# Kernel optimization log

Hardware: AMD Instinct MI355X
Metric: run time of the kernel (lower is better)

Reference implementation:

```python
import jax, jax.numpy as jnp
import numpy as np

B, S, D, H = 32, 1024, 512, 512  # batch, seq_len, input_size, hidden_size


def _init_dir_params(key, D, H):
    # Gate order along the stacked 4H axis: i, f, o, c (matches NaiveLSTM gates)
    k = jax.random.split(key, 4)
    s_in = 1.0 / np.sqrt(D)
    s_h = 1.0 / np.sqrt(H)
    Wx = jax.random.uniform(k[0], (4 * H, D), jnp.float32, -s_in, s_in)
    Wh = jax.random.uniform(k[1], (4 * H, H), jnp.float32, -s_h, s_h)
    bx = jax.random.uniform(k[2], (4 * H,), jnp.float32, -s_in, s_in)
    bh = jax.random.uniform(k[3], (4 * H,), jnp.float32, -s_h, s_h)
    # torch code sets W_f.bias and U_f.bias to 1.0 (forget-gate slice = index 1)
    bx = bx.at[H:2 * H].set(1.0)
    bh = bh.at[H:2 * H].set(1.0)
    return Wx, Wh, bx, bh


def setup_inputs() -> dict:
    key = jax.random.key(0)
    kx, kf, kb = jax.random.split(key, 3)
    x = jax.random.normal(kx, (B, S, D), jnp.float32)
    Wx_f, Wh_f, bx_f, bh_f = _init_dir_params(kf, D, H)
    Wx_b, Wh_b, bx_b, bh_b = _init_dir_params(kb, D, H)
    return {"x": x, "Wx_f": Wx_f, "Wh_f": Wh_f, "bx_f": bx_f, "bh_f": bh_f,
            "Wx_b": Wx_b, "Wh_b": Wh_b, "bx_b": bx_b, "bh_b": bh_b}


def _run_lstm(x_seq, Wx, Wh, bx, bh):
    # x_seq: [B, S, D]; returns (hs [B,S,H], h_final [B,H], c_final [B,H])
    b = x_seq.shape[0]
    h_dim = Wh.shape[1]
    # one big GEMM for all input-to-hidden projections (fused across gates & time)
    xg = jnp.einsum('bsd,gd->bsg', x_seq, Wx) + bx  # [B, S, 4H]

    def step(carry, xg_t):
        h, c = carry
        g = xg_t + h @ Wh.T + bh  # [B, 4H]
        i, f, o, ct = jnp.split(g, 4, axis=-1)
        c_new = jax.nn.sigmoid(f) * c + jax.nn.sigmoid(i) * jnp.tanh(ct)
        h_new = jax.nn.sigmoid(o) * jnp.tanh(c_new)
        return (h_new, c_new), h_new

    init = (jnp.zeros((b, h_dim), x_seq.dtype), jnp.zeros((b, h_dim), x_seq.dtype))
    (hN, cN), hs = jax.lax.scan(step, init, jnp.swapaxes(xg, 0, 1))
    return jnp.swapaxes(hs, 0, 1), hN, cN


def reference(x, Wx_f, Wh_f, bx_f, bh_f, Wx_b, Wh_b, bx_b, bh_b):
    out_f, hF, cF = _run_lstm(x, Wx_f, Wh_f, bx_f, bh_f)
    # backward direction: scan over time-reversed sequence, then un-reverse
    out_b_rev, hB, cB = _run_lstm(x[:, ::-1], Wx_b, Wh_b, bx_b, bh_b)
    out_b = out_b_rev[:, ::-1]
    outputs = jnp.concatenate([out_f, out_b], axis=-1)  # dropout p=0.0 -> identity
    final_hidden = jnp.concatenate([hF, hB], axis=-1)
    final_cell = jnp.concatenate([cF, cB], axis=-1)
    return outputs, final_hidden, final_cell
```

## Files before the change

kernel.cpp:

```cpp
#include <hip/hip_runtime.h>

typedef unsigned short u16;
typedef unsigned int u32;
typedef unsigned long long u64;
typedef __attribute__((ext_vector_type(8))) short short8v;
typedef __attribute__((ext_vector_type(8))) __bf16 bf16x8;
typedef __attribute__((ext_vector_type(4))) float f32x4;
typedef __attribute__((ext_vector_type(2))) float f32x2;

#define AS1 __attribute__((address_space(1)))
#define AS3 __attribute__((address_space(3)))

__device__ __forceinline__ u16 f2bf(float f) {
  unsigned u = __float_as_uint(f);
  u += 0x7fffu + ((u >> 16) & 1u);
  return (u16)(u >> 16);
}
__device__ __forceinline__ float bf2f(u16 h) {
  return __uint_as_float(((unsigned)h) << 16);
}
__device__ __forceinline__ void gload_lds16(const void* g, void* l) {
  __builtin_amdgcn_global_load_lds((const AS1 void*)g, (AS3 void*)l, 16, 0, 0);
}
__device__ __forceinline__ bf16x8 ld8(const u16* p) {
  return __builtin_bit_cast(bf16x8, *reinterpret_cast<const short8v*>(p));
}
__device__ __forceinline__ float sigf(float x) { return 1.0f / (1.0f + __expf(-x)); }
__device__ __forceinline__ float tanhfast(float x) {
  float e = __expf(2.0f * x);
  return 1.0f - 2.0f / (e + 1.0f);
}

__global__ __launch_bounds__(256) void k_conv_x(const float* __restrict__ x,
                                                u16* __restrict__ xh) {
  int i = blockIdx.x * 256 + threadIdx.x;
  float4 v = reinterpret_cast<const float4*>(x)[i];
  ushort4 o;
  o.x = f2bf(v.x); o.y = f2bf(v.y); o.z = f2bf(v.z); o.w = f2bf(v.w);
  reinterpret_cast<ushort4*>(xh)[i] = o;
}

__global__ __launch_bounds__(256) void k_pack_w(
    const float* __restrict__ Wx_f, const float* __restrict__ Wh_f,
    const float* __restrict__ bx_f, const float* __restrict__ bh_f,
    const float* __restrict__ Wx_b, const float* __restrict__ Wh_b,
    const float* __restrict__ bx_b, const float* __restrict__ bh_b,
    u16* __restrict__ wall, u16* __restrict__ whp, float* __restrict__ bias) {
  int i = blockIdx.x * 256 + threadIdx.x;
  int np = i >> 7;
  int k4 = i & 127;
  int d  = np >> 11;
  int p  = np & 2047;
  int src = (p & 3) * 512 + (p >> 2);
  const float* wx = d ? Wx_b : Wx_f;
  const float* wh = d ? Wh_b : Wh_f;
  float4 vx = reinterpret_cast<const float4*>(wx + (size_t)src * 512)[k4];
  float4 vh = reinterpret_cast<const float4*>(wh + (size_t)src * 512)[k4];
  ushort4 ox, oh;
  ox.x = f2bf(vx.x); ox.y = f2bf(vx.y); ox.z = f2bf(vx.z); ox.w = f2bf(vx.w);
  oh.x = f2bf(vh.x); oh.y = f2bf(vh.y); oh.z = f2bf(vh.z); oh.w = f2bf(vh.w);
  reinterpret_cast<ushort4*>(wall + (size_t)np * 512)[k4] = ox;
  reinterpret_cast<ushort4*>(whp  + (size_t)np * 512)[k4] = oh;
  if (k4 == 0) bias[np] = d ? (bx_b[src] + bh_b[src]) : (bx_f[src] + bh_f[src]);
}

template <bool XGBF16>
__global__ __launch_bounds__(256) void k_gemm_xg(
    const u16* __restrict__ A, const u16* __restrict__ Bw,
    const float* __restrict__ bias,
    float* __restrict__ Cf, u16* __restrict__ Ch) {
  __shared__ __align__(16) u16 lA[128 * 32];
  __shared__ __align__(16) u16 lB[128 * 32];
  const int tid  = threadIdx.x;
  const int lane = tid & 63;
  const int w    = tid >> 6;
  const int wr   = w >> 1, wc = w & 1;
  const size_t brow = (size_t)blockIdx.y * 128;
  const int    bcol = blockIdx.x * 128;

  f32x4 acc[4][4] = {};

  for (int kk = 0; kk < 16; ++kk) {
    const int k0 = kk * 32;
    __syncthreads();
#pragma unroll
    for (int q = 0; q < 2; ++q) {
      int idx = q * 256 + tid;
      int row = idx >> 2, c = idx & 3;
      gload_lds16(A  + (brow + row) * 512 + k0 + c * 8, &lA[idx * 8]);
      gload_lds16(Bw + (size_t)(bcol + row) * 512 + k0 + c * 8, &lB[idx * 8]);
    }
    __syncthreads();

    bf16x8 af[4], bfr[4];
#pragma unroll
    for (int m = 0; m < 4; ++m) {
      int row = wr * 64 + m * 16 + (lane & 15);
      af[m] = ld8(&lA[row * 32 + (lane >> 4) * 8]);
    }
#pragma unroll
    for (int n = 0; n < 4; ++n) {
      int row = wc * 64 + n * 16 + (lane & 15);
      bfr[n] = ld8(&lB[row * 32 + (lane >> 4) * 8]);
    }
#pragma unroll
    for (int m = 0; m < 4; ++m)
#pragma unroll
      for (int n = 0; n < 4; ++n)
        acc[m][n] = __builtin_amdgcn_mfma_f32_16x16x32_bf16(af[m], bfr[n], acc[m][n], 0, 0, 0);
  }

#pragma unroll
  for (int m = 0; m < 4; ++m) {
#pragma unroll
    for (int n = 0; n < 4; ++n) {
      int col = bcol + wc * 64 + n * 16 + (lane & 15);
      float bb = bias[col];
#pragma unroll
      for (int r = 0; r < 4; ++r) {
        size_t row = brow + wr * 64 + m * 16 + (lane >> 4) * 4 + r;
        float v = acc[m][n][r] + bb;
        if (XGBF16) Ch[row * 4096 + col] = f2bf(v);
        else        Cf[row * 4096 + col] = v;
      }
    }
  }
}

template <bool XGBF16>
__global__ __launch_bounds__(256, 1) void k_rnn(
    const u16* __restrict__ whp,
    const float* __restrict__ xgf, const u16* __restrict__ xgh,
    u32* __restrict__ hbuf, u32* __restrict__ flags,
    float* __restrict__ out, float* __restrict__ fh, float* __restrict__ fc) {
  const int tid  = threadIdx.x;
  const int lane = tid & 63;
  const int w    = tid >> 6;
  const int bid  = (int)blockIdx.x;
  const int d     = bid >> 4;
  const int ntile = bid & 15;

  __shared__ __align__(16) u16 hlds[32 * 512];
  __shared__ __align__(16) float gbuf[32][132];

  const u16* wbase = whp + (size_t)(d * 2048 + ntile * 128 + w * 32) * 512;
  bf16x8 wf[16][2];
#pragma unroll
  for (int kk = 0; kk < 16; ++kk)
#pragma unroll
    for (int n = 0; n < 2; ++n)
      wf[kk][n] = ld8(wbase + (size_t)(n * 16 + (lane & 15)) * 512 + kk * 32 + (lane >> 4) * 8);

  const int brow = tid >> 4;
  const int jp   = tid & 15;
  const int colbase = d * 2048 + ntile * 128 + jp * 8;
  const int r0 = lane & 15;
  const int qb = lane >> 4;
  const int swz = r0 & 7;

  float cst[2][2] = {{0.f, 0.f}, {0.f, 0.f}};

  const int FSTR = 64;
  u32* myflag = flags + (d * 16 + ntile) * FSTR;
  const u32* spinflag = flags + (d * 16 + ((tid & 127) >> 3)) * FSTR;

  for (int t = 0; t < 1024; ++t) {
    const int sd = d ? (1023 - t) : t;

    short8v xh0, xh1;
    f32x4 xf0a, xf0b, xf1a, xf1b;
    {
      size_t xoff0 = ((size_t)(brow * 1024 + sd)) * 4096 + colbase;
      size_t xoff1 = ((size_t)((16 + brow) * 1024 + sd)) * 4096 + colbase;
      if (XGBF16) {
        xh0 = *reinterpret_cast<const short8v*>(xgh + xoff0);
        xh1 = *reinterpret_cast<const short8v*>(xgh + xoff1);
      } else {
        xf0a = *reinterpret_cast<const f32x4*>(xgf + xoff0);
        xf0b = *reinterpret_cast<const f32x4*>(xgf + xoff0 + 4);
        xf1a = *reinterpret_cast<const f32x4*>(xgf + xoff1);
        xf1b = *reinterpret_cast<const f32x4*>(xgf + xoff1 + 4);
      }
    }

    if (t > 0) {
      while (__hip_atomic_load(spinflag, __ATOMIC_RELAXED, __HIP_MEMORY_SCOPE_AGENT) < (u32)t)
        __builtin_amdgcn_s_sleep(1);
      asm volatile("" ::: "memory");
    }

    const u64* hg = (const u64*)hbuf + ((size_t)(t & 1) * 2 + d) * 4096;
    u64 hv[16];
#pragma unroll
    for (int p = 0; p < 16; ++p)
      hv[p] = __hip_atomic_load(hg + p * 256 + tid, __ATOMIC_RELAXED, __HIP_MEMORY_SCOPE_AGENT);

    {
      char* hb = (char*)hlds;
#pragma unroll
      for (int p = 0; p < 16; ++p) {
        int idx = p * 256 + tid;
        int b = idx >> 7, jq = idx & 127;
        *(u64*)(hb + b * 1024 + (((jq >> 1) ^ (b & 7)) << 4) + ((jq & 1) << 3)) = hv[p];
      }
    }
    __syncthreads();

    f32x4 acc[2][2] = {};
    {
      const char* hbc = (const char*)hlds;
#pragma unroll
      for (int kk = 0; kk < 16; ++kk) {
        int u0 = (((kk * 4 + qb) ^ swz) << 4);
        bf16x8 a0 = *(const bf16x8*)(hbc + r0 * 1024 + u0);
        bf16x8 a1 = *(const bf16x8*)(hbc + (16 + r0) * 1024 + u0);
#pragma unroll
        for (int n = 0; n < 2; ++n) {
          acc[0][n] = __builtin_amdgcn_mfma_f32_16x16x32_bf16(a0, wf[kk][n], acc[0][n], 0, 0, 0);
          acc[1][n] = __builtin_amdgcn_mfma_f32_16x16x32_bf16(a1, wf[kk][n], acc[1][n], 0, 0, 0);
        }
      }
    }

#pragma unroll
    for (int m = 0; m < 2; ++m)
#pragma unroll
      for (int n = 0; n < 2; ++n)
#pragma unroll
        for (int r = 0; r < 4; ++r)
          gbuf[m * 16 + qb * 4 + r][w * 32 + n * 16 + r0] = acc[m][n][r];
    __syncthreads();

    u32* hdst = hbuf + ((size_t)((t + 1) & 1) * 2 + d) * 8192;
    u32 pk[2];
    float hh[2][2];
#pragma unroll
    for (int it = 0; it < 2; ++it) {
      int b = it * 16 + brow;
      float4 g0 = *reinterpret_cast<const float4*>(&gbuf[b][jp * 8]);
      float4 g1 = *reinterpret_cast<const float4*>(&gbuf[b][jp * 8 + 4]);
      float xi0, xff0, xo0, xc0, xi1, xff1, xo1, xc1;
      if (XGBF16) {
        const short8v& xv = it ? xh1 : xh0;
        xi0 = bf2f((u16)xv[0]); xff0 = bf2f((u16)xv[1]);
        xo0 = bf2f((u16)xv[2]); xc0  = bf2f((u16)xv[3]);
        xi1 = bf2f((u16)xv[4]); xff1 = bf2f((u16)xv[5]);
        xo1 = bf2f((u16)xv[6]); xc1  = bf2f((u16)xv[7]);
      } else {
        const f32x4& va = it ? xf1a : xf0a;
        const f32x4& vb = it ? xf1b : xf0b;
        xi0 = va[0]; xff0 = va[1]; xo0 = va[2]; xc0 = va[3];
        xi1 = vb[0]; xff1 = vb[1]; xo1 = vb[2]; xc1 = vb[3];
      }
      float gi0 = g0.x + xi0, gf0 = g0.y + xff0, go0 = g0.z + xo0, gc0 = g0.w + xc0;
      float gi1 = g1.x + xi1, gf1 = g1.y + xff1, go1 = g1.z + xo1, gc1 = g1.w + xc1;
      float cn0 = sigf(gf0) * cst[it][0] + sigf(gi0) * tanhfast(gc0);
      float cn1 = sigf(gf1) * cst[it][1] + sigf(gi1) * tanhfast(gc1);
      float hn0 = sigf(go0) * tanhfast(cn0);
      float hn1 = sigf(go1) * tanhfast(cn1);
      cst[it][0] = cn0; cst[it][1] = cn1;
      pk[it] = (u32)f2bf(hn0) | ((u32)f2bf(hn1) << 16);
      hh[it][0] = hn0; hh[it][1] = hn1;
    }

#pragma unroll
    for (int it = 0; it < 2; ++it) {
      int b = it * 16 + brow;
      __hip_atomic_store(hdst + b * 256 + ntile * 16 + jp, pk[it],
                         __ATOMIC_RELAXED, __HIP_MEMORY_SCOPE_AGENT);
    }
    asm volatile("s_waitcnt vmcnt(0)" ::: "memory");
    __syncthreads();
    if (tid == 0)
      __hip_atomic_store(myflag, (u32)(t + 1), __ATOMIC_RELAXED, __HIP_MEMORY_SCOPE_AGENT);

#pragma unroll
    for (int it = 0; it < 2; ++it) {
      int b = it * 16 + brow;
      f32x2 ov; ov.x = hh[it][0]; ov.y = hh[it][1];
      __builtin_nontemporal_store(ov, reinterpret_cast<f32x2*>(
          out + ((size_t)(b * 1024 + sd)) * 1024 + d * 512 + ntile * 32 + jp * 2));
      if (t == 1023) {
        int fo = b * 1024 + d * 512 + ntile * 32 + jp * 2;
        f32x2 hv2; hv2.x = hh[it][0]; hv2.y = hh[it][1];
        f32x2 cv2; cv2.x = cst[it][0]; cv2.y = cst[it][1];
        *reinterpret_cast<f32x2*>(fh + fo) = hv2;
        *reinterpret_cast<f32x2*>(fc + fo) = cv2;
      }
    }
  }
}

extern "C" void kernel_launch(void* const* d_in, const int* in_sizes, int n_in,
                              void* d_out, int out_size, void* d_ws, size_t ws_size,
                              hipStream_t stream) {
  (void)in_sizes; (void)n_in; (void)out_size;
  const float* x    = (const float*)d_in[0];
  const float* Wx_f = (const float*)d_in[1];
  const float* Wh_f = (const float*)d_in[2];
  const float* bx_f = (const float*)d_in[3];
  const float* bh_f = (const float*)d_in[4];
  const float* Wx_b = (const float*)d_in[5];
  const float* Wh_b = (const float*)d_in[6];
  const float* bx_b = (const float*)d_in[7];
  const float* bh_b = (const float*)d_in[8];

  char* ws = (char*)d_ws;
  const size_t XG_F32 = (size_t)32768 * 4096 * 4;
  const size_t XG_BF  = (size_t)32768 * 4096 * 2;
  const size_t REST   = 33554432 + 4194304 + 4194304 + 16384 + 262144 + 16384;
  const bool xg_bf16 = (ws_size < XG_F32 + REST);

  size_t off = xg_bf16 ? XG_BF : XG_F32;
  float* xg_f = (float*)ws;
  u16*   xg_h = (u16*)ws;
  u16*   xh   = (u16*)(ws + off);  off += 33554432;
  u16*   wall = (u16*)(ws + off);  off += 4194304;
  u16*   whp  = (u16*)(ws + off);  off += 4194304;
  float* bias = (float*)(ws + off); off += 16384;
  u32*   hbuf = (u32*)(ws + off);  off += 262144;
  u32*   flags = (u32*)(ws + off); off += 16384;

  float* out = (float*)d_out;
  float* fh  = out + (size_t)33554432;
  float* fc  = fh + 32768;

  hipError_t e = hipMemsetAsync(hbuf, 0, 262144 + 16384, stream);
  (void)e;
  k_conv_x<<<16384, 256, 0, stream>>>(x, xh);
  k_pack_w<<<2048, 256, 0, stream>>>(Wx_f, Wh_f, bx_f, bh_f,
                                     Wx_b, Wh_b, bx_b, bh_b, wall, whp, bias);
  if (xg_bf16) {
    k_gemm_xg<true><<<dim3(32, 256), 256, 0, stream>>>(xh, wall, bias, nullptr, xg_h);
    k_rnn<true><<<32, 256, 0, stream>>>(whp, nullptr, xg_h, hbuf, flags, out, fh, fc);
  } else {
    k_gemm_xg<false><<<dim3(32, 256), 256, 0, stream>>>(xh, wall, bias, xg_f, nullptr);
    k_rnn<false><<<32, 256, 0, stream>>>(whp, xg_f, nullptr, hbuf, flags, out, fh, fc);
  }
}
```

Measured before the change: 3.820 ms.

## Replace flag-based step sync with sentinel-valued triple-buffered hidden state polling

Drops the per-block flag counters and instead triple-buffers the hidden state in global memory, filling unwritten slots with a sentinel pattern that consumers poll until every value is valid. Each wave now loads its MFMA A-fragments straight from global memory into registers, which removes the LDS staging and one barrier per step. A producer clears the buffer two steps ahead. The aim is to shorten the per-timestep cross-block handoff latency, at the cost of redundant global reads (each wave reads the full 32x512 h), higher register pressure from 64 u64 values, and a theoretical false sentinel match on a real bf16 pair.

```diff
diff --git a/kernel.cpp b/kernel.cpp
--- a/kernel.cpp
+++ b/kernel.cpp
@@ -7,9 +7,13 @@
 typedef __attribute__((ext_vector_type(8))) __bf16 bf16x8;
 typedef __attribute__((ext_vector_type(4))) float f32x4;
 typedef __attribute__((ext_vector_type(2))) float f32x2;
+typedef __attribute__((ext_vector_type(2))) u64 u64x2;
 
 #define AS1 __attribute__((address_space(1)))
 #define AS3 __attribute__((address_space(3)))
+
+#define SENT32 0x7F7F7F7Fu
+#define SENT64 0x7F7F7F7F7F7F7F7FULL
 
 __device__ __forceinline__ u16 f2bf(float f) {
   unsigned u = __float_as_uint(f);
@@ -131,7 +135,7 @@
 __global__ __launch_bounds__(256, 1) void k_rnn(
     const u16* __restrict__ whp,
     const float* __restrict__ xgf, const u16* __restrict__ xgh,
-    u32* __restrict__ hbuf, u32* __restrict__ flags,
+    u32* __restrict__ hbuf3,
     float* __restrict__ out, float* __restrict__ fh, float* __restrict__ fc) {
   const int tid  = threadIdx.x;
   const int lane = tid & 63;
@@ -140,29 +144,25 @@
   const int d     = bid >> 4;
   const int ntile = bid & 15;
 
-  __shared__ __align__(16) u16 hlds[32 * 512];
   __shared__ __align__(16) float gbuf[32][132];
 
   const u16* wbase = whp + (size_t)(d * 2048 + ntile * 128 + w * 32) * 512;
+  const int r0 = lane & 15;
+  const int qb = lane >> 4;
   bf16x8 wf[16][2];
 #pragma unroll
   for (int kk = 0; kk < 16; ++kk)
 #pragma unroll
     for (int n = 0; n < 2; ++n)
-      wf[kk][n] = ld8(wbase + (size_t)(n * 16 + (lane & 15)) * 512 + kk * 32 + (lane >> 4) * 8);
+      wf[kk][n] = ld8(wbase + (size_t)(n * 16 + r0) * 512 + kk * 32 + qb * 8);
 
   const int brow = tid >> 4;
   const int jp   = tid & 15;
   const int colbase = d * 2048 + ntile * 128 + jp * 8;
-  const int r0 = lane & 15;
-  const int qb = lane >> 4;
-  const int swz = r0 & 7;
 
   float cst[2][2] = {{0.f, 0.f}, {0.f, 0.f}};
 
-  const int FSTR = 64;
-  u32* myflag = flags + (d * 16 + ntile) * FSTR;
-  const u32* spinflag = flags + (d * 16 + ((tid & 127) >> 3)) * FSTR;
+  const int fragbase = r0 * 128 + qb * 2;
 
   for (int t = 0; t < 1024; ++t) {
     const int sd = d ? (1023 - t) : t;
@@ -183,42 +183,47 @@
       }
     }
 
-    if (t > 0) {
-      while (__hip_atomic_load(spinflag, __ATOMIC_RELAXED, __HIP_MEMORY_SCOPE_AGENT) < (u32)t)
-        __builtin_amdgcn_s_sleep(1);
-      asm volatile("" ::: "memory");
-    }
-
-    const u64* hg = (const u64*)hbuf + ((size_t)(t & 1) * 2 + d) * 4096;
-    u64 hv[16];
-#pragma unroll
-    for (int p = 0; p < 16; ++p)
-      hv[p] = __hip_atomic_load(hg + p * 256 + tid, __ATOMIC_RELAXED, __HIP_MEMORY_SCOPE_AGENT);
+    const u64* hb = (const u64*)hbuf3 + ((size_t)(t % 3) * 2 + d) * 4096;
+    u64 hv[64];
+    for (;;) {
+#pragma unroll
+      for (int kk = 0; kk < 16; ++kk) {
+        hv[kk * 2]          = __hip_atomic_load(hb + fragbase + kk * 8,
+                                  __ATOMIC_RELAXED, __HIP_MEMORY_SCOPE_AGENT);
+        hv[kk * 2 + 1]      = __hip_atomic_load(hb + fragbase + kk * 8 + 1,
+                                  __ATOMIC_RELAXED, __HIP_MEMORY_SCOPE_AGENT);
+        hv[32 + kk * 2]     = __hip_atomic_load(hb + 2048 + fragbase + kk * 8,
+                                  __ATOMIC_RELAXED, __HIP_MEMORY_SCOPE_AGENT);
+        hv[32 + kk * 2 + 1] = __hip_atomic_load(hb + 2048 + fragbase + kk * 8 + 1,
+                                  __ATOMIC_RELAXED, __HIP_MEMORY_SCOPE_AGENT);
+      }
+      int ok = 1;
+#pragma unroll
+      for (int i = 0; i < 64; ++i) {
+        u32 lo = (u32)hv[i], hi = (u32)(hv[i] >> 32);
+        ok &= (lo != SENT32) & (hi != SENT32);
+      }
+      if (ok) break;
+      __builtin_amdgcn_s_sleep(1);
+    }
 
     {
-      char* hb = (char*)hlds;
-#pragma unroll
-      for (int p = 0; p < 16; ++p) {
-        int idx = p * 256 + tid;
-        int b = idx >> 7, jq = idx & 127;
-        *(u64*)(hb + b * 1024 + (((jq >> 1) ^ (b & 7)) << 4) + ((jq & 1) << 3)) = hv[p];
-      }
-    }
-    __syncthreads();
+      u64* clr = (u64*)hbuf3 + ((size_t)((t + 2) % 3) * 2 + d) * 4096
+                 + ntile * 256 + tid;
+      __hip_atomic_store(clr, SENT64, __ATOMIC_RELAXED, __HIP_MEMORY_SCOPE_AGENT);
+    }
 
     f32x4 acc[2][2] = {};
-    {
-      const char* hbc = (const char*)hlds;
-#pragma unroll
-      for (int kk = 0; kk < 16; ++kk) {
-        int u0 = (((kk * 4 + qb) ^ swz) << 4);
-        bf16x8 a0 = *(const bf16x8*)(hbc + r0 * 1024 + u0);
-        bf16x8 a1 = *(const bf16x8*)(hbc + (16 + r0) * 1024 + u0);
-#pragma unroll
-        for (int n = 0; n < 2; ++n) {
-          acc[0][n] = __builtin_amdgcn_mfma_f32_16x16x32_bf16(a0, wf[kk][n], acc[0][n], 0, 0, 0);
-          acc[1][n] = __builtin_amdgcn_mfma_f32_16x16x32_bf16(a1, wf[kk][n], acc[1][n], 0, 0, 0);
-        }
+#pragma unroll
+    for (int kk = 0; kk < 16; ++kk) {
+      u64x2 t0; t0[0] = hv[kk * 2];      t0[1] = hv[kk * 2 + 1];
+      u64x2 t1; t1[0] = hv[32 + kk * 2]; t1[1] = hv[32 + kk * 2 + 1];
+      bf16x8 a0 = __builtin_bit_cast(bf16x8, t0);
+      bf16x8 a1 = __builtin_bit_cast(bf16x8, t1);
+#pragma unroll
+      for (int n = 0; n < 2; ++n) {
+        acc[0][n] = __builtin_amdgcn_mfma_f32_16x16x32_bf16(a0, wf[kk][n], acc[0][n], 0, 0, 0);
+        acc[1][n] = __builtin_amdgcn_mfma_f32_16x16x32_bf16(a1, wf[kk][n], acc[1][n], 0, 0, 0);
       }
     }
 
@@ -231,7 +236,6 @@
           gbuf[m * 16 + qb * 4 + r][w * 32 + n * 16 + r0] = acc[m][n][r];
     __syncthreads();
 
-    u32* hdst = hbuf + ((size_t)((t + 1) & 1) * 2 + d) * 8192;
     u32 pk[2];
     float hh[2][2];
 #pragma unroll
@@ -262,17 +266,18 @@
       pk[it] = (u32)f2bf(hn0) | ((u32)f2bf(hn1) << 16);
       hh[it][0] = hn0; hh[it][1] = hn1;
     }
-
-#pragma unroll
-    for (int it = 0; it < 2; ++it) {
-      int b = it * 16 + brow;
-      __hip_atomic_store(hdst + b * 256 + ntile * 16 + jp, pk[it],
-                         __ATOMIC_RELAXED, __HIP_MEMORY_SCOPE_AGENT);
-    }
+    __syncthreads();
+
     asm volatile("s_waitcnt vmcnt(0)" ::: "memory");
-    __syncthreads();
-    if (tid == 0)
-      __hip_atomic_store(myflag, (u32)(t + 1), __ATOMIC_RELAXED, __HIP_MEMORY_SCOPE_AGENT);
+    if (t < 1023) {
+      u32* hdst = hbuf3 + ((size_t)((t + 1) % 3) * 2 + d) * 8192;
+#pragma unroll
+      for (int it = 0; it < 2; ++it) {
+        int b = it * 16 + brow;
+        __hip_atomic_store(hdst + b * 256 + ntile * 16 + jp, pk[it],
+                           __ATOMIC_RELAXED, __HIP_MEMORY_SCOPE_AGENT);
+      }
+    }
 
 #pragma unroll
     for (int it = 0; it < 2; ++it) {
@@ -308,7 +313,7 @@
   char* ws = (char*)d_ws;
   const size_t XG_F32 = (size_t)32768 * 4096 * 4;
   const size_t XG_BF  = (size_t)32768 * 4096 * 2;
-  const size_t REST   = 33554432 + 4194304 + 4194304 + 16384 + 262144 + 16384;
+  const size_t REST   = 33554432 + 4194304 + 4194304 + 16384 + 196608;
   const bool xg_bf16 = (ws_size < XG_F32 + REST);
 
   size_t off = xg_bf16 ? XG_BF : XG_F32;
@@ -318,23 +323,24 @@
   u16*   wall = (u16*)(ws + off);  off += 4194304;
   u16*   whp  = (u16*)(ws + off);  off += 4194304;
   float* bias = (float*)(ws + off); off += 16384;
-  u32*   hbuf = (u32*)(ws + off);  off += 262144;
-  u32*   flags = (u32*)(ws + off); off += 16384;
+  u32*   hbuf3 = (u32*)(ws + off); off += 196608;
 
   float* out = (float*)d_out;
   float* fh  = out + (size_t)33554432;
   float* fc  = fh + 32768;
 
-  hipError_t e = hipMemsetAsync(hbuf, 0, 262144 + 16384, stream);
-  (void)e;
+  hipError_t e;
+  e = hipMemsetAsync(hbuf3, 0, 65536, stream);              (void)e;
+  e = hipMemsetAsync((char*)hbuf3 + 65536, 0x7F, 131072, stream); (void)e;
+
   k_conv_x<<<16384, 256, 0, stream>>>(x, xh);
   k_pack_w<<<2048, 256, 0, stream>>>(Wx_f, Wh_f, bx_f, bh_f,
                                      Wx_b, Wh_b, bx_b, bh_b, wall, whp, bias);
   if (xg_bf16) {
     k_gemm_xg<true><<<dim3(32, 256), 256, 0, stream>>>(xh, wall, bias, nullptr, xg_h);
-    k_rnn<true><<<32, 256, 0, stream>>>(whp, nullptr, xg_h, hbuf, flags, out, fh, fc);
+    k_rnn<true><<<32, 256, 0, stream>>>(whp, nullptr, xg_h, hbuf3, out, fh, fc);
   } else {
     k_gemm_xg<false><<<dim3(32, 256), 256, 0, stream>>>(xh, wall, bias, xg_f, nullptr);
-    k_rnn<false><<<32, 256, 0, stream>>>(whp, xg_f, nullptr, hbuf, flags, out, fh, fc);
+    k_rnn<false><<<32, 256, 0, stream>>>(whp, xg_f, nullptr, hbuf3, out, fh, fc);
   }
 }
```

New measurement: 13.89 ms. 264% more time.

## Load h fragments straight into registers and use per-wave flags for step sync

Applied to the files above, without the earlier changes.

The recurrent kernel no longer stages the hidden state through LDS. Each lane loads its MFMA A-fragments directly from the global h buffer, which removes the LDS write, one barrier and the LDS reads per timestep. Synchronisation now uses one flag per wave instead of one per block: each wave publishes its own flag after its stores drain, and consumers spin with a wave-wide ballot over 64 flags. The cost is more scattered, smaller global loads and more register pressure (64 u64 values per lane), plus a restructured barrier placement.

```diff
diff --git a/kernel.cpp b/kernel.cpp
--- a/kernel.cpp
+++ b/kernel.cpp
@@ -7,6 +7,7 @@
 typedef __attribute__((ext_vector_type(8))) __bf16 bf16x8;
 typedef __attribute__((ext_vector_type(4))) float f32x4;
 typedef __attribute__((ext_vector_type(2))) float f32x2;
+typedef __attribute__((ext_vector_type(2))) u64 u64x2;
 
 #define AS1 __attribute__((address_space(1)))
 #define AS3 __attribute__((address_space(3)))
@@ -140,29 +141,29 @@
   const int d     = bid >> 4;
   const int ntile = bid & 15;
 
-  __shared__ __align__(16) u16 hlds[32 * 512];
   __shared__ __align__(16) float gbuf[32][132];
 
   const u16* wbase = whp + (size_t)(d * 2048 + ntile * 128 + w * 32) * 512;
+  const int r0 = lane & 15;
+  const int qb = lane >> 4;
   bf16x8 wf[16][2];
 #pragma unroll
   for (int kk = 0; kk < 16; ++kk)
 #pragma unroll
     for (int n = 0; n < 2; ++n)
-      wf[kk][n] = ld8(wbase + (size_t)(n * 16 + (lane & 15)) * 512 + kk * 32 + (lane >> 4) * 8);
+      wf[kk][n] = ld8(wbase + (size_t)(n * 16 + r0) * 512 + kk * 32 + qb * 8);
 
   const int brow = tid >> 4;
   const int jp   = tid & 15;
   const int colbase = d * 2048 + ntile * 128 + jp * 8;
-  const int r0 = lane & 15;
-  const int qb = lane >> 4;
-  const int swz = r0 & 7;
 
   float cst[2][2] = {{0.f, 0.f}, {0.f, 0.f}};
 
-  const int FSTR = 64;
-  u32* myflag = flags + (d * 16 + ntile) * FSTR;
-  const u32* spinflag = flags + (d * 16 + ((tid & 127) >> 3)) * FSTR;
+  const int FSTR = 16;
+  u32* myflag = flags + (size_t)(d * 64 + ntile * 4 + w) * FSTR;
+  const u32* spinflag = flags + (size_t)(d * 64 + lane) * FSTR;
+
+  const int fragbase = r0 * 128 + qb * 2;
 
   for (int t = 0; t < 1024; ++t) {
     const int sd = d ? (1023 - t) : t;
@@ -184,41 +185,36 @@
     }
 
     if (t > 0) {
-      while (__hip_atomic_load(spinflag, __ATOMIC_RELAXED, __HIP_MEMORY_SCOPE_AGENT) < (u32)t)
+      for (;;) {
+        u32 v = __hip_atomic_load(spinflag, __ATOMIC_RELAXED, __HIP_MEMORY_SCOPE_AGENT);
+        if (__ballot(v >= (u32)t) == ~0ull) break;
         __builtin_amdgcn_s_sleep(1);
+      }
       asm volatile("" ::: "memory");
     }
 
-    const u64* hg = (const u64*)hbuf + ((size_t)(t & 1) * 2 + d) * 4096;
-    u64 hv[16];
-#pragma unroll
-    for (int p = 0; p < 16; ++p)
-      hv[p] = __hip_atomic_load(hg + p * 256 + tid, __ATOMIC_RELAXED, __HIP_MEMORY_SCOPE_AGENT);
-
-    {
-      char* hb = (char*)hlds;
-#pragma unroll
-      for (int p = 0; p < 16; ++p) {
-        int idx = p * 256 + tid;
-        int b = idx >> 7, jq = idx & 127;
-        *(u64*)(hb + b * 1024 + (((jq >> 1) ^ (b & 7)) << 4) + ((jq & 1) << 3)) = hv[p];
-      }
-    }
-    __syncthreads();
+    const u64* hb = (const u64*)hbuf + ((size_t)(t & 1) * 2 + d) * 4096;
+    u64 hv[64];
+#pragma unroll
+    for (int kk = 0; kk < 16; ++kk) {
+      const u64* p0 = hb + fragbase + kk * 8;
+      hv[kk * 2]          = __hip_atomic_load(p0,     __ATOMIC_RELAXED, __HIP_MEMORY_SCOPE_AGENT);
+      hv[kk * 2 + 1]      = __hip_atomic_load(p0 + 1, __ATOMIC_RELAXED, __HIP_MEMORY_SCOPE_AGENT);
+      hv[32 + kk * 2]     = __hip_atomic_load(p0 + 2048,     __ATOMIC_RELAXED, __HIP_MEMORY_SCOPE_AGENT);
+      hv[32 + kk * 2 + 1] = __hip_atomic_load(p0 + 2048 + 1, __ATOMIC_RELAXED, __HIP_MEMORY_SCOPE_AGENT);
+    }
 
     f32x4 acc[2][2] = {};
-    {
-      const char* hbc = (const char*)hlds;
-#pragma unroll
-      for (int kk = 0; kk < 16; ++kk) {
-        int u0 = (((kk * 4 + qb) ^ swz) << 4);
-        bf16x8 a0 = *(const bf16x8*)(hbc + r0 * 1024 + u0);
-        bf16x8 a1 = *(const bf16x8*)(hbc + (16 + r0) * 1024 + u0);
-#pragma unroll
-        for (int n = 0; n < 2; ++n) {
-          acc[0][n] = __builtin_amdgcn_mfma_f32_16x16x32_bf16(a0, wf[kk][n], acc[0][n], 0, 0, 0);
-          acc[1][n] = __builtin_amdgcn_mfma_f32_16x16x32_bf16(a1, wf[kk][n], acc[1][n], 0, 0, 0);
-        }
+#pragma unroll
+    for (int kk = 0; kk < 16; ++kk) {
+      u64x2 t0; t0[0] = hv[kk * 2];      t0[1] = hv[kk * 2 + 1];
+      u64x2 t1; t1[0] = hv[32 + kk * 2]; t1[1] = hv[32 + kk * 2 + 1];
+      bf16x8 a0 = __builtin_bit_cast(bf16x8, t0);
+      bf16x8 a1 = __builtin_bit_cast(bf16x8, t1);
+#pragma unroll
+      for (int n = 0; n < 2; ++n) {
+        acc[0][n] = __builtin_amdgcn_mfma_f32_16x16x32_bf16(a0, wf[kk][n], acc[0][n], 0, 0, 0);
+        acc[1][n] = __builtin_amdgcn_mfma_f32_16x16x32_bf16(a1, wf[kk][n], acc[1][n], 0, 0, 0);
       }
     }
 
@@ -231,7 +227,6 @@
           gbuf[m * 16 + qb * 4 + r][w * 32 + n * 16 + r0] = acc[m][n][r];
     __syncthreads();
 
-    u32* hdst = hbuf + ((size_t)((t + 1) & 1) * 2 + d) * 8192;
     u32 pk[2];
     float hh[2][2];
 #pragma unroll
@@ -262,7 +257,9 @@
       pk[it] = (u32)f2bf(hn0) | ((u32)f2bf(hn1) << 16);
       hh[it][0] = hn0; hh[it][1] = hn1;
     }
-
+    __syncthreads();
+
+    u32* hdst = hbuf + ((size_t)((t + 1) & 1) * 2 + d) * 8192;
 #pragma unroll
     for (int it = 0; it < 2; ++it) {
       int b = it * 16 + brow;
@@ -270,8 +267,7 @@
                          __ATOMIC_RELAXED, __HIP_MEMORY_SCOPE_AGENT);
     }
     asm volatile("s_waitcnt vmcnt(0)" ::: "memory");
-    __syncthreads();
-    if (tid == 0)
+    if (lane == 0)
       __hip_atomic_store(myflag, (u32)(t + 1), __ATOMIC_RELAXED, __HIP_MEMORY_SCOPE_AGENT);
 
 #pragma unroll
@@ -308,7 +304,7 @@
   char* ws = (char*)d_ws;
   const size_t XG_F32 = (size_t)32768 * 4096 * 4;
   const size_t XG_BF  = (size_t)32768 * 4096 * 2;
-  const size_t REST   = 33554432 + 4194304 + 4194304 + 16384 + 262144 + 16384;
+  const size_t REST   = 33554432 + 4194304 + 4194304 + 16384 + 262144 + 8192;
   const bool xg_bf16 = (ws_size < XG_F32 + REST);
 
   size_t off = xg_bf16 ? XG_BF : XG_F32;
@@ -319,13 +315,13 @@
   u16*   whp  = (u16*)(ws + off);  off += 4194304;
   float* bias = (float*)(ws + off); off += 16384;
   u32*   hbuf = (u32*)(ws + off);  off += 262144;
-  u32*   flags = (u32*)(ws + off); off += 16384;
+  u32*   flags = (u32*)(ws + off); off += 8192;
 
   float* out = (float*)d_out;
   float* fh  = out + (size_t)33554432;
   float* fc  = fh + 32768;
 
-  hipError_t e = hipMemsetAsync(hbuf, 0, 262144 + 16384, stream);
+  hipError_t e = hipMemsetAsync(hbuf, 0, 262144 + 8192, stream);
   (void)e;
   k_conv_x<<<16384, 256, 0, stream>>>(x, xh);
   k_pack_w<<<2048, 256, 0, stream>>>(Wx_f, Wh_f, bx_f, bh_f,
```

Measured after the change: 9.839 ms. 2.58x slower.

## Replace per-block flag handshake with step-tagged hidden-state words

Applied to the files above, without the earlier changes.

Each bf16 hidden-state pair is now stored as a 64-bit word whose upper half holds the timestep. Consumers spin on the data loads themselves until every tag matches, instead of waiting on a separate flag. This removes the store-drain wait, the extra block barrier and the flag store/poll round trip from the serial recurrence. In exchange, each step moves twice as many bytes of hidden state through global memory, and a failed check re-reads all 32 words.

```diff
diff --git a/kernel.cpp b/kernel.cpp
--- a/kernel.cpp
+++ b/kernel.cpp
@@ -131,7 +131,7 @@
 __global__ __launch_bounds__(256, 1) void k_rnn(
     const u16* __restrict__ whp,
     const float* __restrict__ xgf, const u16* __restrict__ xgh,
-    u32* __restrict__ hbuf, u32* __restrict__ flags,
+    u64* __restrict__ hbuf,
     float* __restrict__ out, float* __restrict__ fh, float* __restrict__ fc) {
   const int tid  = threadIdx.x;
   const int lane = tid & 63;
@@ -144,25 +144,24 @@
   __shared__ __align__(16) float gbuf[32][132];
 
   const u16* wbase = whp + (size_t)(d * 2048 + ntile * 128 + w * 32) * 512;
+  const int r0 = lane & 15;
+  const int qb = lane >> 4;
   bf16x8 wf[16][2];
 #pragma unroll
   for (int kk = 0; kk < 16; ++kk)
 #pragma unroll
     for (int n = 0; n < 2; ++n)
-      wf[kk][n] = ld8(wbase + (size_t)(n * 16 + (lane & 15)) * 512 + kk * 32 + (lane >> 4) * 8);
+      wf[kk][n] = ld8(wbase + (size_t)(n * 16 + r0) * 512 + kk * 32 + qb * 8);
 
   const int brow = tid >> 4;
   const int jp   = tid & 15;
   const int colbase = d * 2048 + ntile * 128 + jp * 8;
-  const int r0 = lane & 15;
-  const int qb = lane >> 4;
   const int swz = r0 & 7;
 
+  const int c16 = (tid >> 4) * 4 + ((tid >> 2) & 3);
+  const int o4  = (tid & 3) * 4;
+
   float cst[2][2] = {{0.f, 0.f}, {0.f, 0.f}};
-
-  const int FSTR = 64;
-  u32* myflag = flags + (d * 16 + ntile) * FSTR;
-  const u32* spinflag = flags + (d * 16 + ((tid & 127) >> 3)) * FSTR;
 
   for (int t = 0; t < 1024; ++t) {
     const int sd = d ? (1023 - t) : t;
@@ -183,26 +182,27 @@
       }
     }
 
-    if (t > 0) {
-      while (__hip_atomic_load(spinflag, __ATOMIC_RELAXED, __HIP_MEMORY_SCOPE_AGENT) < (u32)t)
-        __builtin_amdgcn_s_sleep(1);
-      asm volatile("" ::: "memory");
-    }
-
-    const u64* hg = (const u64*)hbuf + ((size_t)(t & 1) * 2 + d) * 4096;
-    u64 hv[16];
-#pragma unroll
-    for (int p = 0; p < 16; ++p)
-      hv[p] = __hip_atomic_load(hg + p * 256 + tid, __ATOMIC_RELAXED, __HIP_MEMORY_SCOPE_AGENT);
+    const u64* hb = hbuf + ((size_t)(t & 1) * 2 + d) * 8192;
+    u64 hv[32];
+    for (;;) {
+#pragma unroll
+      for (int r = 0; r < 32; ++r)
+        hv[r] = __hip_atomic_load(hb + r * 256 + tid,
+                                  __ATOMIC_RELAXED, __HIP_MEMORY_SCOPE_AGENT);
+      u32 bad = 0;
+#pragma unroll
+      for (int r = 0; r < 32; ++r)
+        bad |= ((u32)(hv[r] >> 32)) ^ (u32)t;
+      if (!bad) break;
+      __builtin_amdgcn_s_sleep(1);
+    }
+    asm volatile("" ::: "memory");
 
     {
-      char* hb = (char*)hlds;
-#pragma unroll
-      for (int p = 0; p < 16; ++p) {
-        int idx = p * 256 + tid;
-        int b = idx >> 7, jq = idx & 127;
-        *(u64*)(hb + b * 1024 + (((jq >> 1) ^ (b & 7)) << 4) + ((jq & 1) << 3)) = hv[p];
-      }
+      char* hby = (char*)hlds;
+#pragma unroll
+      for (int r = 0; r < 32; ++r)
+        *(u32*)(hby + r * 1024 + (size_t)((c16 ^ (r & 7)) << 4) + o4) = (u32)hv[r];
     }
     __syncthreads();
 
@@ -231,7 +231,6 @@
           gbuf[m * 16 + qb * 4 + r][w * 32 + n * 16 + r0] = acc[m][n][r];
     __syncthreads();
 
-    u32* hdst = hbuf + ((size_t)((t + 1) & 1) * 2 + d) * 8192;
     u32 pk[2];
     float hh[2][2];
 #pragma unroll
@@ -263,16 +262,16 @@
       hh[it][0] = hn0; hh[it][1] = hn1;
     }
 
-#pragma unroll
-    for (int it = 0; it < 2; ++it) {
-      int b = it * 16 + brow;
-      __hip_atomic_store(hdst + b * 256 + ntile * 16 + jp, pk[it],
-                         __ATOMIC_RELAXED, __HIP_MEMORY_SCOPE_AGENT);
-    }
-    asm volatile("s_waitcnt vmcnt(0)" ::: "memory");
-    __syncthreads();
-    if (tid == 0)
-      __hip_atomic_store(myflag, (u32)(t + 1), __ATOMIC_RELAXED, __HIP_MEMORY_SCOPE_AGENT);
+    if (t < 1023) {
+      u64* hd = hbuf + ((size_t)((t + 1) & 1) * 2 + d) * 8192;
+      const u64 tag = ((u64)(u32)(t + 1)) << 32;
+#pragma unroll
+      for (int it = 0; it < 2; ++it) {
+        int b = it * 16 + brow;
+        __hip_atomic_store(hd + b * 256 + ntile * 16 + jp, (u64)pk[it] | tag,
+                           __ATOMIC_RELAXED, __HIP_MEMORY_SCOPE_AGENT);
+      }
+    }
 
 #pragma unroll
     for (int it = 0; it < 2; ++it) {
@@ -308,7 +307,7 @@
   char* ws = (char*)d_ws;
   const size_t XG_F32 = (size_t)32768 * 4096 * 4;
   const size_t XG_BF  = (size_t)32768 * 4096 * 2;
-  const size_t REST   = 33554432 + 4194304 + 4194304 + 16384 + 262144 + 16384;
+  const size_t REST   = 33554432 + 4194304 + 4194304 + 16384 + 262144;
   const bool xg_bf16 = (ws_size < XG_F32 + REST);
 
   size_t off = xg_bf16 ? XG_BF : XG_F32;
@@ -318,23 +317,22 @@
   u16*   wall = (u16*)(ws + off);  off += 4194304;
   u16*   whp  = (u16*)(ws + off);  off += 4194304;
   float* bias = (float*)(ws + off); off += 16384;
-  u32*   hbuf = (u32*)(ws + off);  off += 262144;
-  u32*   flags = (u32*)(ws + off); off += 16384;
+  u64*   hbuf = (u64*)(ws + off);  off += 262144;
 
   float* out = (float*)d_out;
   float* fh  = out + (size_t)33554432;
   float* fc  = fh + 32768;
 
-  hipError_t e = hipMemsetAsync(hbuf, 0, 262144 + 16384, stream);
+  hipError_t e = hipMemsetAsync(hbuf, 0, 262144, stream);
   (void)e;
   k_conv_x<<<16384, 256, 0, stream>>>(x, xh);
   k_pack_w<<<2048, 256, 0, stream>>>(Wx_f, Wh_f, bx_f, bh_f,
                                      Wx_b, Wh_b, bx_b, bh_b, wall, whp, bias);
   if (xg_bf16) {
     k_gemm_xg<true><<<dim3(32, 256), 256, 0, stream>>>(xh, wall, bias, nullptr, xg_h);
-    k_rnn<true><<<32, 256, 0, stream>>>(whp, nullptr, xg_h, hbuf, flags, out, fh, fc);
+    k_rnn<true><<<32, 256, 0, stream>>>(whp, nullptr, xg_h, hbuf, out, fh, fc);
   } else {
     k_gemm_xg<false><<<dim3(32, 256), 256, 0, stream>>>(xh, wall, bias, xg_f, nullptr);
-    k_rnn<false><<<32, 256, 0, stream>>>(whp, xg_f, nullptr, hbuf, flags, out, fh, fc);
+    k_rnn<false><<<32, 256, 0, stream>>>(whp, xg_f, nullptr, hbuf, out, fh, fc);
   }
 }
```

Result: slower. 4.293 ms (+12.4%).
